# Optimization experiments

Measured on AMD Instinct MI355X. Metric: run time of the kernel, lower is better.

The kernel has to match this reference:

```python
import jax, jax.numpy as jnp
import numpy as np

N_RUNS = 10  # neighborhoods_per_batch


def setup_inputs() -> dict:
    key = jax.random.key(0)
    k1, k2, k3 = jax.random.split(key, 3)
    B, U, NN, K = 128, 100000, 100, 500
    features = jax.random.normal(k1, (B, U), dtype=jnp.float32)
    positions = jax.random.uniform(k2, (U, 2), dtype=jnp.float32) * 10.0
    neighborhoods = jax.random.randint(k3, (NN, K), 0, U)
    return {"features": features, "positions": positions, "neighborhoods": neighborhoods}


def reference(features, positions, neighborhoods):
    # choose one random neighborhood per run (torch.randint equivalent, fixed key)
    choice = jax.random.randint(jax.random.key(42), (N_RUNS,), 0, neighborhoods.shape[0])
    idx = neighborhoods[choice]  # [n_runs, K]
    K = idx.shape[1]
    ii, jj = np.tril_indices(K, k=-1)  # strictly lower triangle pairs (i > j)

    def one_run(ind):
        nf = features[:, ind]        # [B, K] gathered neighborhood features
        npos = positions[ind]        # [K, 2]
        # pdist -> distance similarity 1/(d+1) over K*(K-1)/2 pairs
        d = jnp.linalg.norm(npos[ii] - npos[jj], axis=-1)
        dist_sim = 1.0 / (d + 1.0)
        # corrcoef of nf.T: rows are the K units (variables), B observations
        x = nf.T                     # [K, B]
        xc = x - x.mean(axis=1, keepdims=True)
        cov = xc @ xc.T              # [K, K]
        s = jnp.sqrt(jnp.diag(cov))
        corr = cov / (s[:, None] * s[None, :])
        resp_sim = corr[ii, jj]
        # pearson correlation between response and distance similarity vectors
        a = resp_sim - resp_sim.mean()
        b = dist_sim - dist_sim.mean()
        r = (a @ b) / (jnp.linalg.norm(a) * jnp.linalg.norm(b))
        return (1.0 - r) / 2.0

    losses = jax.vmap(one_run)(idx)  # vectorized over n_runs (no Python loop)
    return jnp.mean(losses)
```

## Files before the change

### kernel.cpp

```cpp
#include <hip/hip_runtime.h>
#include <stdint.h>

#define U_DIM 100000
#define B_DIM 128
#define K_DIM 500
#define NRUNS 10
#define KPAD  512
#define NTILEPAIRS 36
#define NPAIRBLOCKS (NTILEPAIRS * NRUNS)

struct ChoiceArgs { int c[NRUNS]; };

__global__ __launch_bounds__(256) void prep_kernel(
    const float* __restrict__ feat, const float* __restrict__ pos,
    const int* __restrict__ neigh, float* __restrict__ xn,
    float2* __restrict__ npos, double* __restrict__ accum,
    unsigned* __restrict__ done, ChoiceArgs ch)
{
  if (blockIdx.x == 0) {
    if (threadIdx.x < NRUNS * 5) accum[threadIdx.x] = 0.0;
    if (threadIdx.x == NRUNS * 5) *done = 0u;
  }

  int gw   = (blockIdx.x * 256 + threadIdx.x) >> 6;
  int lane = threadIdx.x & 63;
  if (gw >= NRUNS * K_DIM) return;
  int r = gw / K_DIM;
  int k = gw - r * K_DIM;

  int ind = neigh[ch.c[r] * K_DIM + k];
  float f0 = feat[(size_t)lane        * U_DIM + ind];
  float f1 = feat[(size_t)(lane + 64) * U_DIM + ind];

  float s = f0 + f1;
  #pragma unroll
  for (int off = 32; off; off >>= 1) s += __shfl_xor(s, off);
  float mean = s * (1.0f / 128.0f);

  float a0 = f0 - mean, a1 = f1 - mean;
  float q = a0 * a0 + a1 * a1;
  #pragma unroll
  for (int off = 32; off; off >>= 1) q += __shfl_xor(q, off);
  float inv = rsqrtf(q);

  size_t base = ((size_t)r * KPAD + k) * B_DIM;
  xn[base + lane]      = a0 * inv;
  xn[base + lane + 64] = a1 * inv;
  if (lane == 0) npos[r * KPAD + k] = make_float2(pos[2 * ind], pos[2 * ind + 1]);
}

#define SA 132
#define SB 68

__global__ __launch_bounds__(256) void pair_kernel(
    const float* __restrict__ xn, const float2* __restrict__ npos,
    double* __restrict__ accum, unsigned* __restrict__ done,
    float* __restrict__ out)
{
  __shared__ float  ldsA[64 * SA];
  __shared__ float  ldsBT[128 * SB];
  __shared__ float2 posA[64], posB[64];
  __shared__ float  red[4][5];
  __shared__ bool   isLast;

  int r = blockIdx.y;
  int p = blockIdx.x;
  int ti = 0;
  while ((ti + 1) * (ti + 2) / 2 <= p) ti++;
  int tj = p - ti * (ti + 1) / 2;

  const float*  xr = xn   + (size_t)r * KPAD * B_DIM;
  const float2* pr = npos + r * KPAD;
  int tid = threadIdx.x;

  #pragma unroll
  for (int it = 0; it < 8; it++) {
    int idx = (it * 256 + tid) * 4;
    int row = idx >> 7, col = idx & 127;
    int gi = ti * 64 + row;
    float4 v = (gi < K_DIM) ? *(const float4*)(xr + (size_t)gi * B_DIM + col)
                            : make_float4(0.f, 0.f, 0.f, 0.f);
    *(float4*)(&ldsA[row * SA + col]) = v;
  }
  {
    int j  = tid & 63;
    int bq = (tid >> 6) * 4;
    int gj = tj * 64 + j;
    bool ok = (gj < K_DIM);
    const float* src = xr + (size_t)(ok ? gj : 0) * B_DIM;
    #pragma unroll
    for (int c = 0; c < 128; c += 16) {
      int b = c + bq;
      float4 f = ok ? *(const float4*)(src + b) : make_float4(0.f, 0.f, 0.f, 0.f);
      ldsBT[(b + 0) * SB + j] = f.x;
      ldsBT[(b + 1) * SB + j] = f.y;
      ldsBT[(b + 2) * SB + j] = f.z;
      ldsBT[(b + 3) * SB + j] = f.w;
    }
  }
  if (tid < 64) {
    int gi = ti * 64 + tid;
    posA[tid] = (gi < K_DIM) ? pr[gi] : make_float2(0.f, 0.f);
  } else if (tid < 128) {
    int j = tid - 64, gj = tj * 64 + j;
    posB[j] = (gj < K_DIM) ? pr[gj] : make_float2(0.f, 0.f);
  }
  __syncthreads();

  int tx = tid & 15, ty = tid >> 4;
  float acc[4][4] = {};
  const float* Ap = &ldsA[(ty * 4) * SA];
  const float* Bp = &ldsBT[tx * 4];

  for (int b = 0; b < 128; b += 4) {
    float4 av0 = *(const float4*)(Ap + 0 * SA + b);
    float4 av1 = *(const float4*)(Ap + 1 * SA + b);
    float4 av2 = *(const float4*)(Ap + 2 * SA + b);
    float4 av3 = *(const float4*)(Ap + 3 * SA + b);
    float4 bv0 = *(const float4*)(Bp + (b + 0) * SB);
    float4 bv1 = *(const float4*)(Bp + (b + 1) * SB);
    float4 bv2 = *(const float4*)(Bp + (b + 2) * SB);
    float4 bv3 = *(const float4*)(Bp + (b + 3) * SB);
    float4 av[4] = {av0, av1, av2, av3};
    #pragma unroll
    for (int u = 0; u < 4; ++u) {
      float4 a = av[u];
      acc[u][0] += a.x * bv0.x + a.y * bv1.x + a.z * bv2.x + a.w * bv3.x;
      acc[u][1] += a.x * bv0.y + a.y * bv1.y + a.z * bv2.y + a.w * bv3.y;
      acc[u][2] += a.x * bv0.z + a.y * bv1.z + a.z * bv2.z + a.w * bv3.z;
      acc[u][3] += a.x * bv0.w + a.y * bv1.w + a.z * bv2.w + a.w * bv3.w;
    }
  }

  float sa = 0.f, sb = 0.f, saa = 0.f, sbb = 0.f, sab = 0.f;
  float2 pa[4], pb[4];
  #pragma unroll
  for (int u = 0; u < 4; u++) pa[u] = posA[ty * 4 + u];
  #pragma unroll
  for (int v = 0; v < 4; v++) pb[v] = posB[tx * 4 + v];
  int gi0 = ti * 64 + ty * 4, gj0 = tj * 64 + tx * 4;
  #pragma unroll
  for (int u = 0; u < 4; u++) {
    #pragma unroll
    for (int v = 0; v < 4; v++) {
      int gi = gi0 + u, gj = gj0 + v;
      if (gi < K_DIM && gj < K_DIM && gi > gj) {
        float resp = acc[u][v];
        float dx = pa[u].x - pb[v].x, dy = pa[u].y - pb[v].y;
        float ds = 1.0f / (sqrtf(dx * dx + dy * dy) + 1.0f);
        sa += resp; sb += ds;
        saa += resp * resp; sbb += ds * ds; sab += resp * ds;
      }
    }
  }
  #pragma unroll
  for (int off = 32; off; off >>= 1) {
    sa  += __shfl_xor(sa,  off);
    sb  += __shfl_xor(sb,  off);
    saa += __shfl_xor(saa, off);
    sbb += __shfl_xor(sbb, off);
    sab += __shfl_xor(sab, off);
  }
  int w = tid >> 6;
  if ((tid & 63) == 0) {
    red[w][0] = sa; red[w][1] = sb; red[w][2] = saa; red[w][3] = sbb; red[w][4] = sab;
  }
  __syncthreads();
  if (tid == 0) {
    #pragma unroll
    for (int i = 0; i < 5; i++) {
      double t = (double)red[0][i] + (double)red[1][i] + (double)red[2][i] + (double)red[3][i];
      atomicAdd(&accum[r * 5 + i], t);
    }
    __threadfence();
    unsigned old = atomicAdd(done, 1u);
    isLast = (old == NPAIRBLOCKS - 1);
  }
  __syncthreads();

  if (isLast && tid == 0) {
    const double n = (double)(K_DIM * (K_DIM - 1) / 2);
    double total = 0.0;
    for (int rr_ = 0; rr_ < NRUNS; rr_++) {
      double sa_  = atomicAdd(&accum[rr_ * 5 + 0], 0.0);
      double sb_  = atomicAdd(&accum[rr_ * 5 + 1], 0.0);
      double saa_ = atomicAdd(&accum[rr_ * 5 + 2], 0.0);
      double sbb_ = atomicAdd(&accum[rr_ * 5 + 3], 0.0);
      double sab_ = atomicAdd(&accum[rr_ * 5 + 4], 0.0);
      double cov = sab_ - sa_ * sb_ / n;
      double va  = saa_ - sa_ * sa_ / n;
      double vb  = sbb_ - sb_ * sb_ / n;
      double rv  = cov / sqrt(va * vb);
      total += (1.0 - rv) * 0.5;
    }
    out[0] = (float)(total / NRUNS);
  }
}

static inline uint32_t rotl32_host(uint32_t x, int r) { return (x << r) | (x >> (32 - r)); }

static void tf2x32(uint32_t k0, uint32_t k1, uint32_t c0, uint32_t c1,
                   uint32_t& o0, uint32_t& o1)
{
  const uint32_t rots[2][4] = {{13, 15, 26, 6}, {17, 29, 16, 24}};
  uint32_t ks[3] = {k0, k1, k0 ^ k1 ^ 0x1BD11BDAu};
  uint32_t x0 = c0 + ks[0], x1 = c1 + ks[1];
  for (int i = 0; i < 5; i++) {
    const uint32_t* rr = rots[i & 1];
    for (int j = 0; j < 4; j++) {
      x0 += x1;
      x1 = rotl32_host(x1, (int)rr[j]);
      x1 ^= x0;
    }
    x0 += ks[(i + 1) % 3];
    x1 += ks[(i + 2) % 3] + (uint32_t)(i + 1);
  }
  o0 = x0; o1 = x1;
}

extern "C" void kernel_launch(void* const* d_in, const int* in_sizes, int n_in,
                              void* d_out, int out_size, void* d_ws, size_t ws_size,
                              hipStream_t stream)
{
  const float* feat  = (const float*)d_in[0];
  const float* pos   = (const float*)d_in[1];
  const int*   neigh = (const int*)d_in[2];
  float* out = (float*)d_out;

  ChoiceArgs ch;
  uint32_t A0, B0, A1, B1;
  tf2x32(0u, 42u, 0u, 2u, A0, B0);
  tf2x32(0u, 42u, 1u, 3u, A1, B1);
  uint32_t hi[NRUNS], lo[NRUNS];
  for (int e = 0; e < 5; e++) {
    uint32_t h0, h1, l0, l1;
    tf2x32(A0, A1, (uint32_t)e, (uint32_t)(e + 5), h0, h1);
    hi[e] = h0; hi[e + 5] = h1;
    tf2x32(B0, B1, (uint32_t)e, (uint32_t)(e + 5), l0, l1);
    lo[e] = l0; lo[e + 5] = l1;
  }
  for (int e = 0; e < NRUNS; e++)
    ch.c[e] = (int)(((hi[e] % 100u) * 96u + (lo[e] % 100u)) % 100u);

  char* ws = (char*)d_ws;
  float*  xn    = (float*)ws;
  float2* npos  = (float2*)(ws + (size_t)NRUNS * KPAD * B_DIM * 4);
  double* accum = (double*)(ws + (size_t)NRUNS * KPAD * B_DIM * 4
                               + (size_t)NRUNS * KPAD * 8);
  unsigned* done = (unsigned*)(accum + NRUNS * 5);

  prep_kernel<<<dim3((NRUNS * K_DIM) / 4), 256, 0, stream>>>(feat, pos, neigh, xn, npos, accum, done, ch);
  pair_kernel<<<dim3(NTILEPAIRS, NRUNS), 256, 0, stream>>>(xn, npos, accum, done, out);
}
```

Baseline: 127.7 us.

## Compute correlation tiles with bf16 MFMA per wave instead of FP32 LDS GEMM

Stores the normalized, centered features as bf16 and computes each 32x32 correlation tile with one wavefront issuing 16x16x32 bf16 MFMA instructions that read operands directly from global memory, replacing the 64x64 FP32 LDS-tiled block GEMM. Each wave now owns one tile pair and does its own atomic accumulation, which removes LDS staging and block-level syncs and gives many more independent work units. In exchange, precision of the correlation values drops to bf16 inputs, and there are more double atomics on the accumulators.

```diff
diff --git a/kernel.cpp b/kernel.cpp
--- a/kernel.cpp
+++ b/kernel.cpp
@@ -1,4 +1,5 @@
 #include <hip/hip_runtime.h>
+#include <hip/hip_bf16.h>
 #include <stdint.h>
 
 #define U_DIM 100000
@@ -6,14 +7,19 @@
 #define K_DIM 500
 #define NRUNS 10
 #define KPAD  512
-#define NTILEPAIRS 36
-#define NPAIRBLOCKS (NTILEPAIRS * NRUNS)
+#define TILE  32
+#define NTILES 16
+#define NTILEPAIRS (NTILES * (NTILES + 1) / 2)
+#define NPAIRWAVES (NTILEPAIRS * NRUNS)
+
+typedef __attribute__((ext_vector_type(8))) short short8;
+typedef __attribute__((ext_vector_type(4))) float f32x4;
 
 struct ChoiceArgs { int c[NRUNS]; };
 
 __global__ __launch_bounds__(256) void prep_kernel(
     const float* __restrict__ feat, const float* __restrict__ pos,
-    const int* __restrict__ neigh, float* __restrict__ xn,
+    const int* __restrict__ neigh, __hip_bfloat16* __restrict__ xnb,
     float2* __restrict__ npos, double* __restrict__ accum,
     unsigned* __restrict__ done, ChoiceArgs ch)
 {
@@ -44,115 +50,74 @@
   float inv = rsqrtf(q);
 
   size_t base = ((size_t)r * KPAD + k) * B_DIM;
-  xn[base + lane]      = a0 * inv;
-  xn[base + lane + 64] = a1 * inv;
+  xnb[base + lane]      = __float2bfloat16(a0 * inv);
+  xnb[base + lane + 64] = __float2bfloat16(a1 * inv);
   if (lane == 0) npos[r * KPAD + k] = make_float2(pos[2 * ind], pos[2 * ind + 1]);
 }
 
-#define SA 132
-#define SB 68
-
 __global__ __launch_bounds__(256) void pair_kernel(
-    const float* __restrict__ xn, const float2* __restrict__ npos,
+    const __hip_bfloat16* __restrict__ xnb, const float2* __restrict__ npos,
     double* __restrict__ accum, unsigned* __restrict__ done,
     float* __restrict__ out)
 {
-  __shared__ float  ldsA[64 * SA];
-  __shared__ float  ldsBT[128 * SB];
-  __shared__ float2 posA[64], posB[64];
-  __shared__ float  red[4][5];
-  __shared__ bool   isLast;
-
-  int r = blockIdx.y;
-  int p = blockIdx.x;
+  int gw   = (blockIdx.x * 256 + threadIdx.x) >> 6;
+  int lane = threadIdx.x & 63;
+  if (gw >= NPAIRWAVES) return;
+
+  int r = gw / NTILEPAIRS;
+  int p = gw - r * NTILEPAIRS;
   int ti = 0;
   while ((ti + 1) * (ti + 2) / 2 <= p) ti++;
   int tj = p - ti * (ti + 1) / 2;
-
-  const float*  xr = xn   + (size_t)r * KPAD * B_DIM;
+  int i0 = ti * TILE, j0 = tj * TILE;
+
+  const __hip_bfloat16* xr = xnb + (size_t)r * KPAD * B_DIM;
+  int quad = lane >> 4, l16 = lane & 15;
+
+  f32x4 acc00 = {}, acc01 = {}, acc10 = {}, acc11 = {};
+
+  #pragma unroll
+  for (int kk = 0; kk < 4; kk++) {
+    int kb = kk * 32 + quad * 8;
+    short8 a0 = *(const short8*)(xr + (size_t)(i0 + l16)      * B_DIM + kb);
+    short8 a1 = *(const short8*)(xr + (size_t)(i0 + 16 + l16) * B_DIM + kb);
+    short8 b0 = *(const short8*)(xr + (size_t)(j0 + l16)      * B_DIM + kb);
+    short8 b1 = *(const short8*)(xr + (size_t)(j0 + 16 + l16) * B_DIM + kb);
+    acc00 = __builtin_amdgcn_mfma_f32_16x16x32_bf16(a0, b0, acc00, 0, 0, 0);
+    acc01 = __builtin_amdgcn_mfma_f32_16x16x32_bf16(a0, b1, acc01, 0, 0, 0);
+    acc10 = __builtin_amdgcn_mfma_f32_16x16x32_bf16(a1, b0, acc10, 0, 0, 0);
+    acc11 = __builtin_amdgcn_mfma_f32_16x16x32_bf16(a1, b1, acc11, 0, 0, 0);
+  }
+
   const float2* pr = npos + r * KPAD;
-  int tid = threadIdx.x;
-
-  #pragma unroll
-  for (int it = 0; it < 8; it++) {
-    int idx = (it * 256 + tid) * 4;
-    int row = idx >> 7, col = idx & 127;
-    int gi = ti * 64 + row;
-    float4 v = (gi < K_DIM) ? *(const float4*)(xr + (size_t)gi * B_DIM + col)
-                            : make_float4(0.f, 0.f, 0.f, 0.f);
-    *(float4*)(&ldsA[row * SA + col]) = v;
-  }
-  {
-    int j  = tid & 63;
-    int bq = (tid >> 6) * 4;
-    int gj = tj * 64 + j;
-    bool ok = (gj < K_DIM);
-    const float* src = xr + (size_t)(ok ? gj : 0) * B_DIM;
+  float sa = 0.f, sb = 0.f, saa = 0.f, sbb = 0.f, sab = 0.f;
+
+  int gj0v = j0 + l16, gj1v = j0 + 16 + l16;
+  float2 pj0 = pr[(gj0v < K_DIM) ? gj0v : 0];
+  float2 pj1 = pr[(gj1v < K_DIM) ? gj1v : 0];
+
+  #pragma unroll
+  for (int tis = 0; tis < 2; tis++) {
     #pragma unroll
-    for (int c = 0; c < 128; c += 16) {
-      int b = c + bq;
-      float4 f = ok ? *(const float4*)(src + b) : make_float4(0.f, 0.f, 0.f, 0.f);
-      ldsBT[(b + 0) * SB + j] = f.x;
-      ldsBT[(b + 1) * SB + j] = f.y;
-      ldsBT[(b + 2) * SB + j] = f.z;
-      ldsBT[(b + 3) * SB + j] = f.w;
-    }
-  }
-  if (tid < 64) {
-    int gi = ti * 64 + tid;
-    posA[tid] = (gi < K_DIM) ? pr[gi] : make_float2(0.f, 0.f);
-  } else if (tid < 128) {
-    int j = tid - 64, gj = tj * 64 + j;
-    posB[j] = (gj < K_DIM) ? pr[gj] : make_float2(0.f, 0.f);
-  }
-  __syncthreads();
-
-  int tx = tid & 15, ty = tid >> 4;
-  float acc[4][4] = {};
-  const float* Ap = &ldsA[(ty * 4) * SA];
-  const float* Bp = &ldsBT[tx * 4];
-
-  for (int b = 0; b < 128; b += 4) {
-    float4 av0 = *(const float4*)(Ap + 0 * SA + b);
-    float4 av1 = *(const float4*)(Ap + 1 * SA + b);
-    float4 av2 = *(const float4*)(Ap + 2 * SA + b);
-    float4 av3 = *(const float4*)(Ap + 3 * SA + b);
-    float4 bv0 = *(const float4*)(Bp + (b + 0) * SB);
-    float4 bv1 = *(const float4*)(Bp + (b + 1) * SB);
-    float4 bv2 = *(const float4*)(Bp + (b + 2) * SB);
-    float4 bv3 = *(const float4*)(Bp + (b + 3) * SB);
-    float4 av[4] = {av0, av1, av2, av3};
-    #pragma unroll
-    for (int u = 0; u < 4; ++u) {
-      float4 a = av[u];
-      acc[u][0] += a.x * bv0.x + a.y * bv1.x + a.z * bv2.x + a.w * bv3.x;
-      acc[u][1] += a.x * bv0.y + a.y * bv1.y + a.z * bv2.y + a.w * bv3.y;
-      acc[u][2] += a.x * bv0.z + a.y * bv1.z + a.z * bv2.z + a.w * bv3.z;
-      acc[u][3] += a.x * bv0.w + a.y * bv1.w + a.z * bv2.w + a.w * bv3.w;
-    }
-  }
-
-  float sa = 0.f, sb = 0.f, saa = 0.f, sbb = 0.f, sab = 0.f;
-  float2 pa[4], pb[4];
-  #pragma unroll
-  for (int u = 0; u < 4; u++) pa[u] = posA[ty * 4 + u];
-  #pragma unroll
-  for (int v = 0; v < 4; v++) pb[v] = posB[tx * 4 + v];
-  int gi0 = ti * 64 + ty * 4, gj0 = tj * 64 + tx * 4;
-  #pragma unroll
-  for (int u = 0; u < 4; u++) {
-    #pragma unroll
-    for (int v = 0; v < 4; v++) {
-      int gi = gi0 + u, gj = gj0 + v;
-      if (gi < K_DIM && gj < K_DIM && gi > gj) {
-        float resp = acc[u][v];
-        float dx = pa[u].x - pb[v].x, dy = pa[u].y - pb[v].y;
+    for (int reg = 0; reg < 4; reg++) {
+      int gi = i0 + tis * 16 + quad * 4 + reg;
+      if (gi >= K_DIM) continue;
+      float2 pi = pr[gi];
+      if (gj0v < K_DIM && gi > gj0v) {
+        float resp = tis ? acc10[reg] : acc00[reg];
+        float dx = pi.x - pj0.x, dy = pi.y - pj0.y;
         float ds = 1.0f / (sqrtf(dx * dx + dy * dy) + 1.0f);
-        sa += resp; sb += ds;
-        saa += resp * resp; sbb += ds * ds; sab += resp * ds;
+        sa += resp; sb += ds; saa += resp * resp; sbb += ds * ds; sab += resp * ds;
+      }
+      if (gj1v < K_DIM && gi > gj1v) {
+        float resp = tis ? acc11[reg] : acc01[reg];
+        float dx = pi.x - pj1.x, dy = pi.y - pj1.y;
+        float ds = 1.0f / (sqrtf(dx * dx + dy * dy) + 1.0f);
+        sa += resp; sb += ds; saa += resp * resp; sbb += ds * ds; sab += resp * ds;
       }
     }
   }
+
   #pragma unroll
   for (int off = 32; off; off >>= 1) {
     sa  += __shfl_xor(sa,  off);
@@ -161,39 +126,32 @@
     sbb += __shfl_xor(sbb, off);
     sab += __shfl_xor(sab, off);
   }
-  int w = tid >> 6;
-  if ((tid & 63) == 0) {
-    red[w][0] = sa; red[w][1] = sb; red[w][2] = saa; red[w][3] = sbb; red[w][4] = sab;
-  }
-  __syncthreads();
-  if (tid == 0) {
-    #pragma unroll
-    for (int i = 0; i < 5; i++) {
-      double t = (double)red[0][i] + (double)red[1][i] + (double)red[2][i] + (double)red[3][i];
-      atomicAdd(&accum[r * 5 + i], t);
-    }
+
+  if (lane == 0) {
+    atomicAdd(&accum[r * 5 + 0], (double)sa);
+    atomicAdd(&accum[r * 5 + 1], (double)sb);
+    atomicAdd(&accum[r * 5 + 2], (double)saa);
+    atomicAdd(&accum[r * 5 + 3], (double)sbb);
+    atomicAdd(&accum[r * 5 + 4], (double)sab);
     __threadfence();
     unsigned old = atomicAdd(done, 1u);
-    isLast = (old == NPAIRBLOCKS - 1);
-  }
-  __syncthreads();
-
-  if (isLast && tid == 0) {
-    const double n = (double)(K_DIM * (K_DIM - 1) / 2);
-    double total = 0.0;
-    for (int rr_ = 0; rr_ < NRUNS; rr_++) {
-      double sa_  = atomicAdd(&accum[rr_ * 5 + 0], 0.0);
-      double sb_  = atomicAdd(&accum[rr_ * 5 + 1], 0.0);
-      double saa_ = atomicAdd(&accum[rr_ * 5 + 2], 0.0);
-      double sbb_ = atomicAdd(&accum[rr_ * 5 + 3], 0.0);
-      double sab_ = atomicAdd(&accum[rr_ * 5 + 4], 0.0);
-      double cov = sab_ - sa_ * sb_ / n;
-      double va  = saa_ - sa_ * sa_ / n;
-      double vb  = sbb_ - sb_ * sb_ / n;
-      double rv  = cov / sqrt(va * vb);
-      total += (1.0 - rv) * 0.5;
+    if (old == NPAIRWAVES - 1) {
+      const double n = (double)(K_DIM * (K_DIM - 1) / 2);
+      double total = 0.0;
+      for (int rr_ = 0; rr_ < NRUNS; rr_++) {
+        double sa_  = atomicAdd(&accum[rr_ * 5 + 0], 0.0);
+        double sb_  = atomicAdd(&accum[rr_ * 5 + 1], 0.0);
+        double saa_ = atomicAdd(&accum[rr_ * 5 + 2], 0.0);
+        double sbb_ = atomicAdd(&accum[rr_ * 5 + 3], 0.0);
+        double sab_ = atomicAdd(&accum[rr_ * 5 + 4], 0.0);
+        double cov = sab_ - sa_ * sb_ / n;
+        double va  = saa_ - sa_ * sa_ / n;
+        double vb  = sbb_ - sb_ * sb_ / n;
+        double rv  = cov / sqrt(va * vb);
+        total += (1.0 - rv) * 0.5;
+      }
+      out[0] = (float)(total / NRUNS);
     }
-    out[0] = (float)(total / NRUNS);
   }
 }
 
@@ -243,12 +201,12 @@
     ch.c[e] = (int)(((hi[e] % 100u) * 96u + (lo[e] % 100u)) % 100u);
 
   char* ws = (char*)d_ws;
-  float*  xn    = (float*)ws;
-  float2* npos  = (float2*)(ws + (size_t)NRUNS * KPAD * B_DIM * 4);
-  double* accum = (double*)(ws + (size_t)NRUNS * KPAD * B_DIM * 4
-                               + (size_t)NRUNS * KPAD * 8);
+  __hip_bfloat16* xnb = (__hip_bfloat16*)ws;
+  size_t off0 = (size_t)NRUNS * KPAD * B_DIM * sizeof(__hip_bfloat16);
+  float2* npos  = (float2*)(ws + off0);
+  double* accum = (double*)(ws + off0 + (size_t)NRUNS * KPAD * sizeof(float2));
   unsigned* done = (unsigned*)(accum + NRUNS * 5);
 
-  prep_kernel<<<dim3((NRUNS * K_DIM) / 4), 256, 0, stream>>>(feat, pos, neigh, xn, npos, accum, done, ch);
-  pair_kernel<<<dim3(NTILEPAIRS, NRUNS), 256, 0, stream>>>(xn, npos, accum, done, out);
-}
+  prep_kernel<<<dim3((NRUNS * K_DIM) / 4), 256, 0, stream>>>(feat, pos, neigh, xnb, npos, accum, done, ch);
+  pair_kernel<<<dim3(NPAIRWAVES / 4), 256, 0, stream>>>(xnb, npos, accum, done, out);
+}
```

New measurement: 148.9 us. 1.17x slower.
